# Kernel optimization log

Hardware: AMD Instinct MI355X
Metric: run time of the kernel (lower is better)

Reference implementation:

```python
import jax, jax.numpy as jnp
import numpy as np

B, L, D_PAIR, N_HEAD = 1, 320, 128, 4
EPS = 1e-5


def setup_inputs() -> dict:
    key = jax.random.key(0)
    ks = jax.random.split(key, 8)
    s = 0.05  # ~xavier scale for fan_in=128
    return {
        "pair": jax.random.normal(ks[0], (B, L, L, D_PAIR), jnp.float32),
        "norm_w": jnp.ones((D_PAIR,), jnp.float32),
        "norm_b": jnp.zeros((D_PAIR,), jnp.float32),
        "Wq": jax.random.normal(ks[1], (D_PAIR, D_PAIR), jnp.float32) * s,
        "Wk": jax.random.normal(ks[2], (D_PAIR, D_PAIR), jnp.float32) * s,
        "Wv": jax.random.normal(ks[3], (D_PAIR, D_PAIR), jnp.float32) * s,
        "Wg": jax.random.normal(ks[4], (D_PAIR, D_PAIR), jnp.float32) * s,
        "bg": jnp.zeros((D_PAIR,), jnp.float32),
        "Wo": jax.random.normal(ks[5], (D_PAIR, D_PAIR), jnp.float32) * s,
        "bo": jnp.zeros((D_PAIR,), jnp.float32),
        "Wb": jax.random.normal(ks[6], (N_HEAD, D_PAIR), jnp.float32) * s,
    }


def reference(pair, norm_w, norm_b, Wq, Wk, Wv, Wg, bg, Wo, bo, Wb):
    # Triangle attention, mode='start' (no permute). pair: (B, L, L, D)
    Bs, Ls, _, D = pair.shape
    H = Wb.shape[0]
    Dh = D // H
    scale = Dh ** -0.5

    # LayerNorm (fp32, matches torch eps=1e-5)
    mu = jnp.mean(pair, axis=-1, keepdims=True)
    var = jnp.var(pair, axis=-1, keepdims=True)
    x = (pair - mu) * jax.lax.rsqrt(var + EPS) * norm_w + norm_b

    def heads(y):
        # (B,L,L,D) -> (B,L,H,L,Dh): attention runs along the second L axis per row i
        return y.reshape(Bs, Ls, Ls, H, Dh).transpose(0, 1, 3, 2, 4)

    Q = heads(x @ Wq.T)
    K = heads(x @ Wk.T)
    V = heads(x @ Wv.T)
    g = heads(jax.nn.sigmoid(x @ Wg.T + bg))

    attn = jnp.einsum('blhid,blhjd->blhij', Q, K) * scale  # (B,L,H,L,L)
    # bias from RAW pair (pre-norm), projected to heads, broadcast over query index i
    bias = (pair @ Wb.T).transpose(0, 1, 3, 2)[:, :, :, None, :]  # (B,L,H,1,L)
    attn = jax.nn.softmax(attn + bias, axis=-1)

    out = jnp.einsum('blhij,blhjd->blhid', attn, V)  # (B,L,H,L,Dh)
    out = (g * out).transpose(0, 1, 3, 2, 4).reshape(Bs, Ls, Ls, D)
    return pair + out @ Wo.T + bo
```

## Files before the change

kernel.cpp:

```cpp
#include <hip/hip_runtime.h>

typedef unsigned short u16;
typedef unsigned int u32;
typedef __attribute__((ext_vector_type(8))) short bf16x8;
typedef __attribute__((ext_vector_type(4))) float f32x4;
typedef __attribute__((ext_vector_type(2))) unsigned int u32x2;

#define LOG2E 1.4426950408889634f

__device__ __forceinline__ u16 f2bf(float f) {
    u32 u = __float_as_uint(f);
    u += 0x7fffu + ((u >> 16) & 1u);
    return (u16)(u >> 16);
}
__device__ __forceinline__ u32 pk_bf_trunc(float hi, float lo) {
    return __builtin_amdgcn_perm(__float_as_uint(hi), __float_as_uint(lo), 0x07060302u);
}

__global__ void wconv_kernel(const float* __restrict__ Wq, const float* __restrict__ Wk,
                             const float* __restrict__ Wv, const float* __restrict__ Wg,
                             const float* __restrict__ Wo, const float* __restrict__ norm_w,
                             const float* __restrict__ norm_b, const float* __restrict__ bg,
                             u16* __restrict__ wbf, float* __restrict__ cvec) {
    int b = blockIdx.x;
    if (b < 64) {
        int idx = b * 256 + threadIdx.x;
        float w = norm_w[idx & 127];
        wbf[0 * 16384 + idx] = f2bf(Wq[idx] * w);
        wbf[1 * 16384 + idx] = f2bf(Wk[idx] * w);
        wbf[2 * 16384 + idx] = f2bf(Wv[idx] * w);
        wbf[3 * 16384 + idx] = f2bf(Wg[idx] * w);
        wbf[4 * 16384 + idx] = f2bf(Wo[idx]);
    } else {
        int m = b - 64;
        int n = threadIdx.x;
        if (n < 128) {
            const float* W = (m == 0) ? Wq : (m == 1) ? Wk : (m == 2) ? Wv : Wg;
            float c = 0.f;
#pragma unroll
            for (int k4 = 0; k4 < 32; ++k4) {
                f32x4 bb = *(const f32x4*)&norm_b[k4 * 4];
                f32x4 ww = *(const f32x4*)&W[n * 128 + k4 * 4];
                c += bb[0] * ww[0] + bb[1] * ww[1] + bb[2] * ww[2] + bb[3] * ww[3];
            }
            if (m == 3) c += bg[n];
            cvec[m * 128 + n] = c;
        }
    }
}

#define KS_OFF 9216
#define VTS_OFF 22016
#define PB_W 1152

__global__ __launch_bounds__(512, 4)
void attn_kernel(const float* __restrict__ pair,
                 const float* __restrict__ Wb,
                 const u16* __restrict__ wbf,
                 const float* __restrict__ cvec,
                 u16* __restrict__ Obf,
                 u16* __restrict__ Gg) {
    const int bid = blockIdx.x;
    const int xcd = bid & 7;
    const int s_i = bid >> 3;
    const int h = s_i & 3;
    const int l = ((s_i >> 2) << 3) | xcd;
    const int tid = threadIdx.x;
    const int wave = tid >> 6;
    const int lane = tid & 63;
    const int i_lo = lane & 15;
    const int q = lane >> 4;

    __shared__ __align__(16) u16 smem[32576];
    __shared__ __align__(16) float biasLds[320];

    const int row_g = tid >> 3;
    const int c8 = tid & 7;
    const int wrow = (wave & 3) * 16;
    const int nth_flip = wave >> 2;

    f32x4 wbv[4];
#pragma unroll
    for (int u = 0; u < 4; ++u)
        wbv[u] = *(const f32x4*)&Wb[h * 128 + c8 * 16 + u * 4];

    float cQ[2], cK[2], cV[2], cG[2];
#pragma unroll
    for (int half = 0; half < 2; ++half) {
        int n = h * 32 + half * 16 + i_lo;
        cQ[half] = cvec[0 * 128 + n];
        cK[half] = cvec[1 * 128 + n];
        cV[half] = cvec[2 * 128 + n];
        cG[half] = cvec[3 * 128 + n];
    }

    u32 qkeep[3][4];

#pragma unroll 1
    for (int t = 0; t < 5; ++t) {
        const int j0 = t * 64;
        const float* prow = pair + ((size_t)(l * 320 + j0 + row_g)) * 128 + c8 * 16;
        f32x4 pr[4];
#pragma unroll
        for (int u = 0; u < 4; ++u) pr[u] = *(const f32x4*)(prow + u * 4);

        float s = 0.f, s2 = 0.f, bd = 0.f;
#pragma unroll
        for (int u = 0; u < 4; ++u) {
            f32x4 p = pr[u];
            f32x4 wb4 = wbv[u];
            s += p[0] + p[1] + p[2] + p[3];
            s2 += p[0] * p[0] + p[1] * p[1] + p[2] * p[2] + p[3] * p[3];
            bd += p[0] * wb4[0] + p[1] * wb4[1] + p[2] * wb4[2] + p[3] * wb4[3];
        }
        s += __shfl_xor(s, 1);   s += __shfl_xor(s, 2);   s += __shfl_xor(s, 4);
        s2 += __shfl_xor(s2, 1); s2 += __shfl_xor(s2, 2); s2 += __shfl_xor(s2, 4);
        bd += __shfl_xor(bd, 1); bd += __shfl_xor(bd, 2); bd += __shfl_xor(bd, 4);
        float mu = s * 0.0078125f;
        float var = s2 * 0.0078125f - mu * mu;
        float rs = rsqrtf(var + 1e-5f);

        __syncthreads();
#pragma unroll
        for (int u = 0; u < 4; ++u) {
            f32x4 p = pr[u];
            ushort4 xv;
            xv.x = f2bf((p[0] - mu) * rs);
            xv.y = f2bf((p[1] - mu) * rs);
            xv.z = f2bf((p[2] - mu) * rs);
            xv.w = f2bf((p[3] - mu) * rs);
            *(ushort4*)&smem[row_g * 136 + c8 * 16 + u * 4] = xv;
        }
        if (c8 == 0) biasLds[j0 + row_g] = bd * LOG2E;
        __syncthreads();

        const int nth = (t & 1) ^ nth_flip;
        f32x4 acc[4];
#pragma unroll
        for (int n2 = 0; n2 < 4; ++n2) acc[n2] = (f32x4){0.f, 0.f, 0.f, 0.f};
#pragma unroll
        for (int kc = 0; kc < 4; ++kc) {
            bf16x8 a = *(const bf16x8*)&smem[(wrow + i_lo) * 136 + kc * 32 + q * 8];
#pragma unroll
            for (int n2 = 0; n2 < 4; ++n2) {
                int nt = nth * 4 + n2;
                bf16x8 wf = *(const bf16x8*)&wbf[(nt >> 1) * 16384 +
                                                 (h * 32 + (nt & 1) * 16 + i_lo) * 128 + kc * 32 + q * 8];
                acc[n2] = __builtin_amdgcn_mfma_f32_16x16x32_bf16(a, wf, acc[n2], 0, 0, 0);
            }
        }
        const int jrow = j0 + wrow + q * 4;
        if (nth == 0) {
            const int ti = t >> 1;
#pragma unroll
            for (int dd = 0; dd < 2; ++dd)
#pragma unroll
                for (int rr = 0; rr < 2; ++rr)
                    qkeep[ti][dd * 2 + rr] =
                        (u32)f2bf(acc[dd][rr * 2] + cQ[dd]) |
                        ((u32)f2bf(acc[dd][rr * 2 + 1] + cQ[dd]) << 16);
#pragma unroll
            for (int n2 = 2; n2 < 4; ++n2)
#pragma unroll
                for (int r = 0; r < 4; ++r)
                    smem[KS_OFF + (jrow + r) * 40 + (n2 & 1) * 16 + i_lo] =
                        f2bf(acc[n2][r] + cK[n2 & 1]);
        } else {
#pragma unroll
            for (int n2 = 0; n2 < 2; ++n2)
#pragma unroll
                for (int r = 0; r < 4; ++r)
                    smem[VTS_OFF + (n2 * 16 + i_lo) * 330 + jrow + r] =
                        f2bf(acc[n2][r] + cV[n2]);
#pragma unroll
            for (int n2 = 2; n2 < 4; ++n2)
#pragma unroll
                for (int r = 0; r < 4; ++r) {
                    float z = acc[n2][r] + cG[n2 & 1];
                    float g = 1.0f / (1.0f + exp2f(-z * LOG2E));
                    Gg[((size_t)((l * 4 + h) * 320 + jrow + r)) * 32 + (n2 & 1) * 16 + i_lo] = f2bf(g);
                }
        }
    }
    __syncthreads();

    const float SC = 0.17677669529663687f * LOG2E;
    const f32x4 zero4 = {0.f, 0.f, 0.f, 0.f};
    union { bf16x8 v; u32 u[4]; } onesf;
#pragma unroll
    for (int u = 0; u < 4; ++u) onesf.u[u] = 0x3F803F80u;
    u16* pb = smem + wave * PB_W;
    const int nstrip = (wave < 4) ? 3 : 2;
#pragma unroll 1
    for (int t2 = 0; t2 < nstrip; ++t2) {
        const int i0 = (wave + 8 * t2) * 16;
#pragma unroll
        for (int dd = 0; dd < 2; ++dd)
#pragma unroll
            for (int rr = 0; rr < 2; ++rr) {
                u32 v = qkeep[t2][dd * 2 + rr];
                pb[(q * 4 + rr * 2) * 40 + dd * 16 + i_lo] = (u16)v;
                pb[(q * 4 + rr * 2 + 1) * 40 + dd * 16 + i_lo] = (u16)(v >> 16);
            }
        bf16x8 qf = *(const bf16x8*)&pb[i_lo * 40 + q * 8];

        f32x4 oacc[2];
        oacc[0] = zero4; oacc[1] = zero4;
        f32x4 sacc = zero4;
#pragma unroll 1
        for (int c = 0; c < 5; ++c) {
            f32x4 sc4[4];
#pragma unroll
            for (int jt = 0; jt < 4; ++jt) {
                bf16x8 kf = *(const bf16x8*)&smem[KS_OFF + (c * 64 + jt * 16 + i_lo) * 40 + q * 8];
                sc4[jt] = __builtin_amdgcn_mfma_f32_16x16x32_bf16(kf, qf, zero4, 0, 0, 0);
            }
#pragma unroll
            for (int jt = 0; jt < 4; ++jt) {
                f32x4 b4 = *(const f32x4*)&biasLds[c * 64 + jt * 16 + q * 4];
#pragma unroll
                for (int r = 0; r < 4; ++r)
                    sc4[jt][r] = exp2f(sc4[jt][r] * SC + b4[r]);
            }
#pragma unroll
            for (int jt = 0; jt < 4; ++jt) {
                u32x2 pk;
                pk.x = pk_bf_trunc(sc4[jt][1], sc4[jt][0]);
                pk.y = pk_bf_trunc(sc4[jt][3], sc4[jt][2]);
                *(u32x2*)&pb[i_lo * 72 + jt * 16 + q * 4] = pk;
            }
#pragma unroll
            for (int kt2 = 0; kt2 < 2; ++kt2) {
                bf16x8 pf = *(const bf16x8*)&pb[i_lo * 72 + kt2 * 32 + q * 8];
                sacc = __builtin_amdgcn_mfma_f32_16x16x32_bf16(onesf.v, pf, sacc, 0, 0, 0);
#pragma unroll
                for (int mt = 0; mt < 2; ++mt) {
                    bf16x8 vf = *(const bf16x8*)&smem[VTS_OFF + (mt * 16 + i_lo) * 330 +
                                                      c * 64 + kt2 * 32 + q * 8];
                    oacc[mt] = __builtin_amdgcn_mfma_f32_16x16x32_bf16(vf, pf, oacc[mt], 0, 0, 0);
                }
            }
        }
        float rinv = 1.0f / sacc[0];
#pragma unroll
        for (int mt = 0; mt < 2; ++mt) {
            u32x2 pk;
            pk.x = pk_bf_trunc(oacc[mt][1] * rinv, oacc[mt][0] * rinv);
            pk.y = pk_bf_trunc(oacc[mt][3] * rinv, oacc[mt][2] * rinv);
            *(u32x2*)&Obf[((size_t)(l * 320 + i0 + i_lo)) * 128 + h * 32 + mt * 16 + q * 4] = pk;
        }
    }
}

__global__ __launch_bounds__(256, 4)
void outproj_kernel(const float* __restrict__ pair,
                    const float* __restrict__ bo,
                    const u16* __restrict__ Obf,
                    const u16* __restrict__ Gg,
                    const u16* __restrict__ wbf,
                    float* __restrict__ out) {
    const int tid = threadIdx.x;
    const int wave = tid >> 6;
    const int lane = tid & 63;
    const int i_lo = lane & 15;
    const int q = lane >> 4;

    __shared__ __align__(16) u16 WoLds[128 * 128];

    const int row0 = blockIdx.x * 64 + wave * 16;
    const int lidx = row0 / 320;
    const int irow = row0 - lidx * 320 + i_lo;

    union { bf16x8 v; u32 u[4]; } A[4], G[4];
#pragma unroll
    for (int kc = 0; kc < 4; ++kc) {
        A[kc].v = *(const bf16x8*)&Obf[((size_t)(row0 + i_lo)) * 128 + kc * 32 + q * 8];
        G[kc].v = *(const bf16x8*)&Gg[((size_t)((lidx * 4 + kc) * 320 + irow)) * 32 + q * 8];
    }

    const u16* Wo = wbf + 4 * 16384;
#pragma unroll
    for (int it = 0; it < 8; ++it) {
        int unit = it * 256 + tid;
        int n = unit >> 4, k8 = unit & 15;
        *(bf16x8*)&WoLds[n * 128 + ((k8 ^ (n & 15)) * 8)] = *(const bf16x8*)&Wo[unit * 8];
    }
    __syncthreads();

    bf16x8 of[4];
#pragma unroll
    for (int kc = 0; kc < 4; ++kc) {
        union { bf16x8 v; u32 u[4]; } R;
#pragma unroll
        for (int k4 = 0; k4 < 4; ++k4) {
            float lo = __uint_as_float(A[kc].u[k4] << 16) * __uint_as_float(G[kc].u[k4] << 16);
            float hi = __uint_as_float(A[kc].u[k4] & 0xffff0000u) * __uint_as_float(G[kc].u[k4] & 0xffff0000u);
            R.u[k4] = pk_bf_trunc(hi, lo);
        }
        of[kc] = R.v;
    }

    f32x4 acc[8];
#pragma unroll
    for (int nt = 0; nt < 8; ++nt) acc[nt] = (f32x4){0.f, 0.f, 0.f, 0.f};
#pragma unroll
    for (int nt = 0; nt < 8; ++nt) {
#pragma unroll
        for (int kc = 0; kc < 4; ++kc) {
            bf16x8 wf = *(const bf16x8*)&WoLds[(nt * 16 + i_lo) * 128 + (((kc * 4 + q) ^ i_lo) * 8)];
            acc[nt] = __builtin_amdgcn_mfma_f32_16x16x32_bf16(wf, of[kc], acc[nt], 0, 0, 0);
        }
    }
#pragma unroll
    for (int nt = 0; nt < 8; ++nt) {
        size_t idx = ((size_t)(row0 + i_lo)) * 128 + nt * 16 + q * 4;
        f32x4 p4 = *(const f32x4*)&pair[idx];
        f32x4 b4 = *(const f32x4*)&bo[nt * 16 + q * 4];
        f32x4 o4;
        o4[0] = acc[nt][0] + p4[0] + b4[0];
        o4[1] = acc[nt][1] + p4[1] + b4[1];
        o4[2] = acc[nt][2] + p4[2] + b4[2];
        o4[3] = acc[nt][3] + p4[3] + b4[3];
        *(f32x4*)&out[idx] = o4;
    }
}

extern "C" void kernel_launch(void* const* d_in, const int* in_sizes, int n_in,
                              void* d_out, int out_size, void* d_ws, size_t ws_size,
                              hipStream_t stream) {
    const float* pair   = (const float*)d_in[0];
    const float* norm_w = (const float*)d_in[1];
    const float* norm_b = (const float*)d_in[2];
    const float* Wq     = (const float*)d_in[3];
    const float* Wk     = (const float*)d_in[4];
    const float* Wv     = (const float*)d_in[5];
    const float* Wg     = (const float*)d_in[6];
    const float* bg     = (const float*)d_in[7];
    const float* Wo     = (const float*)d_in[8];
    const float* bo     = (const float*)d_in[9];
    const float* Wb     = (const float*)d_in[10];

    u16* wbf    = (u16*)d_ws;
    float* cvec = (float*)(wbf + 5 * 16384);
    u16* Obf    = (u16*)(cvec + 512);
    u16* Gg     = Obf + (size_t)102400 * 128;
    float* out  = (float*)d_out;

    wconv_kernel<<<68, 256, 0, stream>>>(Wq, Wk, Wv, Wg, Wo, norm_w, norm_b, bg, wbf, cvec);
    attn_kernel<<<320 * 4, 512, 0, stream>>>(pair, Wb, wbf, cvec, Obf, Gg);
    outproj_kernel<<<1600, 256, 0, stream>>>(pair, bo, Obf, Gg, wbf, out);
}
```

Before: 279.4 us.

## Process two query strips per wave sharing K/V fragments; prefetch pair residual in outproj

The attention loop now handles two 16-row query strips at once in each wave. The K fragments, bias and V fragments are loaded once and reused for both strips, and MFMA priority is raised with s_setprio so the second strip's softmax work can overlap the first strip's matrix ops. The third strip, which only waves 0-3 have, stays on the old single-strip path. In the output projection kernel the pair residual is loaded early, before the Wo LDS fill and GEMM, and launch bounds drop to 3 blocks per CU to make room for the extra registers. The trade is higher register pressure and possible loss of occupancy in exchange for fewer LDS reads and more latency hiding.

Measured after the change: 280.5 us. Within noise of the previous version (+0.4%).

```diff
diff --git a/kernel.cpp b/kernel.cpp
--- a/kernel.cpp
+++ b/kernel.cpp
@@ -190,15 +190,128 @@
 #pragma unroll
     for (int u = 0; u < 4; ++u) onesf.u[u] = 0x3F803F80u;
     u16* pb = smem + wave * PB_W;
-    const int nstrip = (wave < 4) ? 3 : 2;
+
+    {
+        const int i0A = wave * 16;
+        const int i0B = (wave + 8) * 16;
+        bf16x8 qfA, qfB;
+#pragma unroll
+        for (int dd = 0; dd < 2; ++dd)
+#pragma unroll
+            for (int rr = 0; rr < 2; ++rr) {
+                u32 v = qkeep[0][dd * 2 + rr];
+                pb[(q * 4 + rr * 2) * 40 + dd * 16 + i_lo] = (u16)v;
+                pb[(q * 4 + rr * 2 + 1) * 40 + dd * 16 + i_lo] = (u16)(v >> 16);
+            }
+        qfA = *(const bf16x8*)&pb[i_lo * 40 + q * 8];
+#pragma unroll
+        for (int dd = 0; dd < 2; ++dd)
+#pragma unroll
+            for (int rr = 0; rr < 2; ++rr) {
+                u32 v = qkeep[1][dd * 2 + rr];
+                pb[(q * 4 + rr * 2) * 40 + dd * 16 + i_lo] = (u16)v;
+                pb[(q * 4 + rr * 2 + 1) * 40 + dd * 16 + i_lo] = (u16)(v >> 16);
+            }
+        qfB = *(const bf16x8*)&pb[i_lo * 40 + q * 8];
+
+        f32x4 oaccA0 = zero4, oaccA1 = zero4, oaccB0 = zero4, oaccB1 = zero4;
+        f32x4 saccA = zero4, saccB = zero4;
 #pragma unroll 1
-    for (int t2 = 0; t2 < nstrip; ++t2) {
-        const int i0 = (wave + 8 * t2) * 16;
+        for (int c = 0; c < 5; ++c) {
+            bf16x8 kf[4];
+#pragma unroll
+            for (int jt = 0; jt < 4; ++jt)
+                kf[jt] = *(const bf16x8*)&smem[KS_OFF + (c * 64 + jt * 16 + i_lo) * 40 + q * 8];
+            f32x4 sA[4], sB[4];
+#pragma unroll
+            for (int jt = 0; jt < 4; ++jt)
+                sA[jt] = __builtin_amdgcn_mfma_f32_16x16x32_bf16(kf[jt], qfA, zero4, 0, 0, 0);
+#pragma unroll
+            for (int jt = 0; jt < 4; ++jt)
+                sB[jt] = __builtin_amdgcn_mfma_f32_16x16x32_bf16(kf[jt], qfB, zero4, 0, 0, 0);
+            f32x4 b4[4];
+#pragma unroll
+            for (int jt = 0; jt < 4; ++jt)
+                b4[jt] = *(const f32x4*)&biasLds[c * 64 + jt * 16 + q * 4];
+#pragma unroll
+            for (int jt = 0; jt < 4; ++jt)
+#pragma unroll
+                for (int r = 0; r < 4; ++r)
+                    sA[jt][r] = exp2f(sA[jt][r] * SC + b4[jt][r]);
+#pragma unroll
+            for (int jt = 0; jt < 4; ++jt) {
+                u32x2 pk;
+                pk.x = pk_bf_trunc(sA[jt][1], sA[jt][0]);
+                pk.y = pk_bf_trunc(sA[jt][3], sA[jt][2]);
+                *(u32x2*)&pb[i_lo * 72 + jt * 16 + q * 4] = pk;
+            }
+#pragma unroll
+            for (int jt = 0; jt < 4; ++jt)
+#pragma unroll
+                for (int r = 0; r < 4; ++r)
+                    sB[jt][r] = exp2f(sB[jt][r] * SC + b4[jt][r]);
+            u32 pBx[4], pBy[4];
+#pragma unroll
+            for (int jt = 0; jt < 4; ++jt) {
+                pBx[jt] = pk_bf_trunc(sB[jt][1], sB[jt][0]);
+                pBy[jt] = pk_bf_trunc(sB[jt][3], sB[jt][2]);
+            }
+            bf16x8 pfA0 = *(const bf16x8*)&pb[i_lo * 72 + 0 * 32 + q * 8];
+            bf16x8 pfA1 = *(const bf16x8*)&pb[i_lo * 72 + 1 * 32 + q * 8];
+#pragma unroll
+            for (int jt = 0; jt < 4; ++jt) {
+                u32x2 pk;
+                pk.x = pBx[jt];
+                pk.y = pBy[jt];
+                *(u32x2*)&pb[i_lo * 72 + jt * 16 + q * 4] = pk;
+            }
+            bf16x8 pfB0 = *(const bf16x8*)&pb[i_lo * 72 + 0 * 32 + q * 8];
+            bf16x8 pfB1 = *(const bf16x8*)&pb[i_lo * 72 + 1 * 32 + q * 8];
+            bf16x8 vf00 = *(const bf16x8*)&smem[VTS_OFF + (0 * 16 + i_lo) * 330 + c * 64 + 0 * 32 + q * 8];
+            bf16x8 vf01 = *(const bf16x8*)&smem[VTS_OFF + (0 * 16 + i_lo) * 330 + c * 64 + 1 * 32 + q * 8];
+            bf16x8 vf10 = *(const bf16x8*)&smem[VTS_OFF + (1 * 16 + i_lo) * 330 + c * 64 + 0 * 32 + q * 8];
+            bf16x8 vf11 = *(const bf16x8*)&smem[VTS_OFF + (1 * 16 + i_lo) * 330 + c * 64 + 1 * 32 + q * 8];
+            __builtin_amdgcn_s_setprio(1);
+            saccA = __builtin_amdgcn_mfma_f32_16x16x32_bf16(onesf.v, pfA0, saccA, 0, 0, 0);
+            saccA = __builtin_amdgcn_mfma_f32_16x16x32_bf16(onesf.v, pfA1, saccA, 0, 0, 0);
+            oaccA0 = __builtin_amdgcn_mfma_f32_16x16x32_bf16(vf00, pfA0, oaccA0, 0, 0, 0);
+            oaccA0 = __builtin_amdgcn_mfma_f32_16x16x32_bf16(vf01, pfA1, oaccA0, 0, 0, 0);
+            oaccA1 = __builtin_amdgcn_mfma_f32_16x16x32_bf16(vf10, pfA0, oaccA1, 0, 0, 0);
+            oaccA1 = __builtin_amdgcn_mfma_f32_16x16x32_bf16(vf11, pfA1, oaccA1, 0, 0, 0);
+            saccB = __builtin_amdgcn_mfma_f32_16x16x32_bf16(onesf.v, pfB0, saccB, 0, 0, 0);
+            saccB = __builtin_amdgcn_mfma_f32_16x16x32_bf16(onesf.v, pfB1, saccB, 0, 0, 0);
+            oaccB0 = __builtin_amdgcn_mfma_f32_16x16x32_bf16(vf00, pfB0, oaccB0, 0, 0, 0);
+            oaccB0 = __builtin_amdgcn_mfma_f32_16x16x32_bf16(vf01, pfB1, oaccB0, 0, 0, 0);
+            oaccB1 = __builtin_amdgcn_mfma_f32_16x16x32_bf16(vf10, pfB0, oaccB1, 0, 0, 0);
+            oaccB1 = __builtin_amdgcn_mfma_f32_16x16x32_bf16(vf11, pfB1, oaccB1, 0, 0, 0);
+            __builtin_amdgcn_s_setprio(0);
+        }
+        float rinvA = 1.0f / saccA[0];
+        float rinvB = 1.0f / saccB[0];
+        {
+            u32x2 pk;
+            pk.x = pk_bf_trunc(oaccA0[1] * rinvA, oaccA0[0] * rinvA);
+            pk.y = pk_bf_trunc(oaccA0[3] * rinvA, oaccA0[2] * rinvA);
+            *(u32x2*)&Obf[((size_t)(l * 320 + i0A + i_lo)) * 128 + h * 32 + 0 * 16 + q * 4] = pk;
+            pk.x = pk_bf_trunc(oaccA1[1] * rinvA, oaccA1[0] * rinvA);
+            pk.y = pk_bf_trunc(oaccA1[3] * rinvA, oaccA1[2] * rinvA);
+            *(u32x2*)&Obf[((size_t)(l * 320 + i0A + i_lo)) * 128 + h * 32 + 1 * 16 + q * 4] = pk;
+            pk.x = pk_bf_trunc(oaccB0[1] * rinvB, oaccB0[0] * rinvB);
+            pk.y = pk_bf_trunc(oaccB0[3] * rinvB, oaccB0[2] * rinvB);
+            *(u32x2*)&Obf[((size_t)(l * 320 + i0B + i_lo)) * 128 + h * 32 + 0 * 16 + q * 4] = pk;
+            pk.x = pk_bf_trunc(oaccB1[1] * rinvB, oaccB1[0] * rinvB);
+            pk.y = pk_bf_trunc(oaccB1[3] * rinvB, oaccB1[2] * rinvB);
+            *(u32x2*)&Obf[((size_t)(l * 320 + i0B + i_lo)) * 128 + h * 32 + 1 * 16 + q * 4] = pk;
+        }
+    }
+
+    if (wave < 4) {
+        const int i0 = (wave + 16) * 16;
 #pragma unroll
         for (int dd = 0; dd < 2; ++dd)
 #pragma unroll
             for (int rr = 0; rr < 2; ++rr) {
-                u32 v = qkeep[t2][dd * 2 + rr];
+                u32 v = qkeep[2][dd * 2 + rr];
                 pb[(q * 4 + rr * 2) * 40 + dd * 16 + i_lo] = (u16)v;
                 pb[(q * 4 + rr * 2 + 1) * 40 + dd * 16 + i_lo] = (u16)(v >> 16);
             }
@@ -252,7 +365,7 @@
     }
 }
 
-__global__ __launch_bounds__(256, 4)
+__global__ __launch_bounds__(256, 3)
 void outproj_kernel(const float* __restrict__ pair,
                     const float* __restrict__ bo,
                     const u16* __restrict__ Obf,
@@ -277,6 +390,10 @@
         A[kc].v = *(const bf16x8*)&Obf[((size_t)(row0 + i_lo)) * 128 + kc * 32 + q * 8];
         G[kc].v = *(const bf16x8*)&Gg[((size_t)((lidx * 4 + kc) * 320 + irow)) * 32 + q * 8];
     }
+    f32x4 pr[8];
+#pragma unroll
+    for (int nt = 0; nt < 8; ++nt)
+        pr[nt] = *(const f32x4*)&pair[((size_t)(row0 + i_lo)) * 128 + nt * 16 + q * 4];
 
     const u16* Wo = wbf + 4 * 16384;
 #pragma unroll
@@ -314,13 +431,12 @@
 #pragma unroll
     for (int nt = 0; nt < 8; ++nt) {
         size_t idx = ((size_t)(row0 + i_lo)) * 128 + nt * 16 + q * 4;
-        f32x4 p4 = *(const f32x4*)&pair[idx];
         f32x4 b4 = *(const f32x4*)&bo[nt * 16 + q * 4];
         f32x4 o4;
-        o4[0] = acc[nt][0] + p4[0] + b4[0];
-        o4[1] = acc[nt][1] + p4[1] + b4[1];
-        o4[2] = acc[nt][2] + p4[2] + b4[2];
-        o4[3] = acc[nt][3] + p4[3] + b4[3];
+        o4[0] = acc[nt][0] + pr[nt][0] + b4[0];
+        o4[1] = acc[nt][1] + pr[nt][1] + b4[1];
+        o4[2] = acc[nt][2] + pr[nt][2] + b4[2];
+        o4[3] = acc[nt][3] + pr[nt][3] + b4[3];
         *(f32x4*)&out[idx] = o4;
     }
 }
```

## Split fused attention kernel into separate projection and attention kernels

Applied to the files above, without the earlier changes.

Replaces the monolithic per-(row, head) attention kernel with two kernels. A projection kernel LayerNorms pair rows and computes Q, K, V^T, the gate and the bias (the bias now via an MFMA against a padded bf16 Wb), writing them to global scratch and reusing the output buffer for Q and K. A separate attention kernel then runs one 64-query block per workgroup and reads K and V directly from global memory. This removes the redundant per-head LayerNorm of each pair row and raises parallelism and occupancy, at the cost of extra global round-trips for Q, K and V. The output projection also prefetches the residual pair values early.

Result: slower. 365.0 us (+30.6%).

```diff
diff --git a/kernel.cpp b/kernel.cpp
--- a/kernel.cpp
+++ b/kernel.cpp
@@ -7,12 +7,16 @@
 typedef __attribute__((ext_vector_type(2))) unsigned int u32x2;
 
 #define LOG2E 1.4426950408889634f
+#define PB_W 1152
 
 __device__ __forceinline__ u16 f2bf(float f) {
     u32 u = __float_as_uint(f);
     u += 0x7fffu + ((u >> 16) & 1u);
     return (u16)(u >> 16);
 }
+__device__ __forceinline__ u32 pk2(float lo, float hi) {
+    return (u32)f2bf(lo) | ((u32)f2bf(hi) << 16);
+}
 __device__ __forceinline__ u32 pk_bf_trunc(float hi, float lo) {
     return __builtin_amdgcn_perm(__float_as_uint(hi), __float_as_uint(lo), 0x07060302u);
 }
@@ -21,6 +25,7 @@
                              const float* __restrict__ Wv, const float* __restrict__ Wg,
                              const float* __restrict__ Wo, const float* __restrict__ norm_w,
                              const float* __restrict__ norm_b, const float* __restrict__ bg,
+                             const float* __restrict__ Wb,
                              u16* __restrict__ wbf, float* __restrict__ cvec) {
     int b = blockIdx.x;
     if (b < 64) {
@@ -31,7 +36,7 @@
         wbf[2 * 16384 + idx] = f2bf(Wv[idx] * w);
         wbf[3 * 16384 + idx] = f2bf(Wg[idx] * w);
         wbf[4 * 16384 + idx] = f2bf(Wo[idx]);
-    } else {
+    } else if (b < 68) {
         int m = b - 64;
         int n = threadIdx.x;
         if (n < 128) {
@@ -46,213 +51,191 @@
             if (m == 3) c += bg[n];
             cvec[m * 128 + n] = c;
         }
-    }
-}
-
-#define KS_OFF 9216
-#define VTS_OFF 22016
-#define PB_W 1152
-
-__global__ __launch_bounds__(512, 4)
-void attn_kernel(const float* __restrict__ pair,
-                 const float* __restrict__ Wb,
-                 const u16* __restrict__ wbf,
-                 const float* __restrict__ cvec,
-                 u16* __restrict__ Obf,
-                 u16* __restrict__ Gg) {
+    } else {
+#pragma unroll
+        for (int e = 0; e < 8; ++e) {
+            int idx = threadIdx.x * 8 + e;
+            int n = idx >> 7;
+            wbf[5 * 16384 + idx] = (n < 4) ? f2bf(Wb[idx]) : (u16)0;
+        }
+    }
+}
+
+__global__ __launch_bounds__(256, 4)
+void proj_kernel(const float* __restrict__ pair, const u16* __restrict__ wbf,
+                 const float* __restrict__ cvec, u16* __restrict__ Qbf,
+                 u16* __restrict__ Ksb, u16* __restrict__ VTb,
+                 u16* __restrict__ Gg, float* __restrict__ biasT) {
     const int bid = blockIdx.x;
     const int xcd = bid & 7;
-    const int s_i = bid >> 3;
-    const int h = s_i & 3;
-    const int l = ((s_i >> 2) << 3) | xcd;
+    const int s = bid >> 3;
+    const int jc = s % 5;
+    const int l = (s / 5) * 8 + xcd;
     const int tid = threadIdx.x;
     const int wave = tid >> 6;
     const int lane = tid & 63;
     const int i_lo = lane & 15;
     const int q = lane >> 4;
-
-    __shared__ __align__(16) u16 smem[32576];
-    __shared__ __align__(16) float biasLds[320];
-
-    const int row_g = tid >> 3;
-    const int c8 = tid & 7;
-    const int wrow = (wave & 3) * 16;
-    const int nth_flip = wave >> 2;
-
-    f32x4 wbv[4];
-#pragma unroll
-    for (int u = 0; u < 4; ++u)
-        wbv[u] = *(const f32x4*)&Wb[h * 128 + c8 * 16 + u * 4];
-
-    float cQ[2], cK[2], cV[2], cG[2];
-#pragma unroll
-    for (int half = 0; half < 2; ++half) {
-        int n = h * 32 + half * 16 + i_lo;
-        cQ[half] = cvec[0 * 128 + n];
-        cK[half] = cvec[1 * 128 + n];
-        cV[half] = cvec[2 * 128 + n];
-        cG[half] = cvec[3 * 128 + n];
-    }
-
-    u32 qkeep[3][4];
+    const int j0 = jc * 64 + wave * 16;
+    const int row = l * 320 + j0 + i_lo;
+    const f32x4 zero4 = {0.f, 0.f, 0.f, 0.f};
+
+    f32x4 pr[8];
+    const float* pp = pair + (size_t)row * 128 + q * 8;
+#pragma unroll
+    for (int kc = 0; kc < 4; ++kc) {
+        pr[kc * 2 + 0] = *(const f32x4*)(pp + kc * 32 + 0);
+        pr[kc * 2 + 1] = *(const f32x4*)(pp + kc * 32 + 4);
+    }
+    float s1 = 0.f, s2 = 0.f;
+#pragma unroll
+    for (int u = 0; u < 8; ++u) {
+        f32x4 p = pr[u];
+        s1 += p[0] + p[1] + p[2] + p[3];
+        s2 += p[0] * p[0] + p[1] * p[1] + p[2] * p[2] + p[3] * p[3];
+    }
+    s1 += __shfl_xor(s1, 16); s1 += __shfl_xor(s1, 32);
+    s2 += __shfl_xor(s2, 16); s2 += __shfl_xor(s2, 32);
+    float mu = s1 * 0.0078125f;
+    float var = s2 * 0.0078125f - mu * mu;
+    float rs = rsqrtf(var + 1e-5f);
+
+    union { bf16x8 v; u32 u[4]; } xa[4], ra[4];
+#pragma unroll
+    for (int kc = 0; kc < 4; ++kc) {
+        f32x4 a = pr[kc * 2 + 0], b = pr[kc * 2 + 1];
+        ra[kc].u[0] = pk2(a[0], a[1]); ra[kc].u[1] = pk2(a[2], a[3]);
+        ra[kc].u[2] = pk2(b[0], b[1]); ra[kc].u[3] = pk2(b[2], b[3]);
+        xa[kc].u[0] = pk2((a[0] - mu) * rs, (a[1] - mu) * rs);
+        xa[kc].u[1] = pk2((a[2] - mu) * rs, (a[3] - mu) * rs);
+        xa[kc].u[2] = pk2((b[0] - mu) * rs, (b[1] - mu) * rs);
+        xa[kc].u[3] = pk2((b[2] - mu) * rs, (b[3] - mu) * rs);
+    }
+
+    f32x4 bacc = zero4;
+#pragma unroll
+    for (int kc = 0; kc < 4; ++kc) {
+        bf16x8 wf = *(const bf16x8*)&wbf[5 * 16384 + i_lo * 128 + kc * 32 + q * 8];
+        bacc = __builtin_amdgcn_mfma_f32_16x16x32_bf16(ra[kc].v, wf, bacc, 0, 0, 0);
+    }
+    if (i_lo < 4) {
+#pragma unroll
+        for (int r = 0; r < 4; ++r)
+            biasT[(size_t)(l * 4 + i_lo) * 320 + j0 + q * 4 + r] = bacc[r] * LOG2E;
+    }
 
 #pragma unroll 1
-    for (int t = 0; t < 5; ++t) {
-        const int j0 = t * 64;
-        const float* prow = pair + ((size_t)(l * 320 + j0 + row_g)) * 128 + c8 * 16;
-        f32x4 pr[4];
-#pragma unroll
-        for (int u = 0; u < 4; ++u) pr[u] = *(const f32x4*)(prow + u * 4);
-
-        float s = 0.f, s2 = 0.f, bd = 0.f;
-#pragma unroll
-        for (int u = 0; u < 4; ++u) {
-            f32x4 p = pr[u];
-            f32x4 wb4 = wbv[u];
-            s += p[0] + p[1] + p[2] + p[3];
-            s2 += p[0] * p[0] + p[1] * p[1] + p[2] * p[2] + p[3] * p[3];
-            bd += p[0] * wb4[0] + p[1] * wb4[1] + p[2] * wb4[2] + p[3] * wb4[3];
-        }
-        s += __shfl_xor(s, 1);   s += __shfl_xor(s, 2);   s += __shfl_xor(s, 4);
-        s2 += __shfl_xor(s2, 1); s2 += __shfl_xor(s2, 2); s2 += __shfl_xor(s2, 4);
-        bd += __shfl_xor(bd, 1); bd += __shfl_xor(bd, 2); bd += __shfl_xor(bd, 4);
-        float mu = s * 0.0078125f;
-        float var = s2 * 0.0078125f - mu * mu;
-        float rs = rsqrtf(var + 1e-5f);
-
-        __syncthreads();
-#pragma unroll
-        for (int u = 0; u < 4; ++u) {
-            f32x4 p = pr[u];
-            ushort4 xv;
-            xv.x = f2bf((p[0] - mu) * rs);
-            xv.y = f2bf((p[1] - mu) * rs);
-            xv.z = f2bf((p[2] - mu) * rs);
-            xv.w = f2bf((p[3] - mu) * rs);
-            *(ushort4*)&smem[row_g * 136 + c8 * 16 + u * 4] = xv;
-        }
-        if (c8 == 0) biasLds[j0 + row_g] = bd * LOG2E;
-        __syncthreads();
-
-        const int nth = (t & 1) ^ nth_flip;
-        f32x4 acc[4];
-#pragma unroll
-        for (int n2 = 0; n2 < 4; ++n2) acc[n2] = (f32x4){0.f, 0.f, 0.f, 0.f};
-#pragma unroll
-        for (int kc = 0; kc < 4; ++kc) {
-            bf16x8 a = *(const bf16x8*)&smem[(wrow + i_lo) * 136 + kc * 32 + q * 8];
-#pragma unroll
-            for (int n2 = 0; n2 < 4; ++n2) {
-                int nt = nth * 4 + n2;
-                bf16x8 wf = *(const bf16x8*)&wbf[(nt >> 1) * 16384 +
-                                                 (h * 32 + (nt & 1) * 16 + i_lo) * 128 + kc * 32 + q * 8];
-                acc[n2] = __builtin_amdgcn_mfma_f32_16x16x32_bf16(a, wf, acc[n2], 0, 0, 0);
+    for (int m = 0; m < 4; ++m) {
+#pragma unroll 1
+        for (int nt = 0; nt < 8; ++nt) {
+            f32x4 acc = zero4;
+#pragma unroll
+            for (int kc = 0; kc < 4; ++kc) {
+                bf16x8 wf = *(const bf16x8*)&wbf[m * 16384 + (nt * 16 + i_lo) * 128 + kc * 32 + q * 8];
+                acc = __builtin_amdgcn_mfma_f32_16x16x32_bf16(xa[kc].v, wf, acc, 0, 0, 0);
             }
-        }
-        const int jrow = j0 + wrow + q * 4;
-        if (nth == 0) {
-            const int ti = t >> 1;
-#pragma unroll
-            for (int dd = 0; dd < 2; ++dd)
-#pragma unroll
-                for (int rr = 0; rr < 2; ++rr)
-                    qkeep[ti][dd * 2 + rr] =
-                        (u32)f2bf(acc[dd][rr * 2] + cQ[dd]) |
-                        ((u32)f2bf(acc[dd][rr * 2 + 1] + cQ[dd]) << 16);
-#pragma unroll
-            for (int n2 = 2; n2 < 4; ++n2)
+            const float cv = cvec[m * 128 + nt * 16 + i_lo];
+            const int h = nt >> 1, half = nt & 1;
+            const size_t hb = (size_t)(l * 4 + h);
+            const int jr = j0 + q * 4;
+            if (m == 0) {
 #pragma unroll
                 for (int r = 0; r < 4; ++r)
-                    smem[KS_OFF + (jrow + r) * 40 + (n2 & 1) * 16 + i_lo] =
-                        f2bf(acc[n2][r] + cK[n2 & 1]);
-        } else {
-#pragma unroll
-            for (int n2 = 0; n2 < 2; ++n2)
+                    Qbf[(hb * 320 + jr + r) * 32 + half * 16 + i_lo] = f2bf(acc[r] + cv);
+            } else if (m == 1) {
 #pragma unroll
                 for (int r = 0; r < 4; ++r)
-                    smem[VTS_OFF + (n2 * 16 + i_lo) * 330 + jrow + r] =
-                        f2bf(acc[n2][r] + cV[n2]);
-#pragma unroll
-            for (int n2 = 2; n2 < 4; ++n2)
+                    Ksb[(hb * 320 + jr + r) * 32 + half * 16 + i_lo] = f2bf(acc[r] + cv);
+            } else if (m == 2) {
+                ushort4 v4;
+                v4.x = f2bf(acc[0] + cv); v4.y = f2bf(acc[1] + cv);
+                v4.z = f2bf(acc[2] + cv); v4.w = f2bf(acc[3] + cv);
+                *(ushort4*)&VTb[(hb * 32 + half * 16 + i_lo) * 320 + jr] = v4;
+            } else {
 #pragma unroll
                 for (int r = 0; r < 4; ++r) {
-                    float z = acc[n2][r] + cG[n2 & 1];
+                    float z = acc[r] + cv;
                     float g = 1.0f / (1.0f + exp2f(-z * LOG2E));
-                    Gg[((size_t)((l * 4 + h) * 320 + jrow + r)) * 32 + (n2 & 1) * 16 + i_lo] = f2bf(g);
+                    Gg[(hb * 320 + jr + r) * 32 + half * 16 + i_lo] = f2bf(g);
                 }
-        }
-    }
-    __syncthreads();
+            }
+        }
+    }
+}
+
+__global__ __launch_bounds__(256, 6)
+void attnB_kernel(const u16* __restrict__ Qbf, const u16* __restrict__ Ksb,
+                  const u16* __restrict__ VTb, const float* __restrict__ biasT,
+                  u16* __restrict__ Obf) {
+    const int bid = blockIdx.x;
+    const int xcd = bid & 7;
+    const int s = bid >> 3;
+    const int g = s % 5;
+    const int h = (s / 5) & 3;
+    const int l = (s / 20) * 8 + xcd;
+    const int tid = threadIdx.x;
+    const int wave = tid >> 6;
+    const int lane = tid & 63;
+    const int i_lo = lane & 15;
+    const int q = lane >> 4;
+    const int i0 = g * 64 + wave * 16;
+    const size_t hb = (size_t)(l * 4 + h);
+
+    __shared__ __align__(16) u16 smem[4608];
+    u16* pb = smem + wave * PB_W;
 
     const float SC = 0.17677669529663687f * LOG2E;
     const f32x4 zero4 = {0.f, 0.f, 0.f, 0.f};
     union { bf16x8 v; u32 u[4]; } onesf;
 #pragma unroll
     for (int u = 0; u < 4; ++u) onesf.u[u] = 0x3F803F80u;
-    u16* pb = smem + wave * PB_W;
-    const int nstrip = (wave < 4) ? 3 : 2;
+
+    bf16x8 qf = *(const bf16x8*)&Qbf[(hb * 320 + i0 + i_lo) * 32 + q * 8];
+
+    f32x4 oacc0 = zero4, oacc1 = zero4, sacc = zero4;
 #pragma unroll 1
-    for (int t2 = 0; t2 < nstrip; ++t2) {
-        const int i0 = (wave + 8 * t2) * 16;
-#pragma unroll
-        for (int dd = 0; dd < 2; ++dd)
-#pragma unroll
-            for (int rr = 0; rr < 2; ++rr) {
-                u32 v = qkeep[t2][dd * 2 + rr];
-                pb[(q * 4 + rr * 2) * 40 + dd * 16 + i_lo] = (u16)v;
-                pb[(q * 4 + rr * 2 + 1) * 40 + dd * 16 + i_lo] = (u16)(v >> 16);
-            }
-        bf16x8 qf = *(const bf16x8*)&pb[i_lo * 40 + q * 8];
-
-        f32x4 oacc[2];
-        oacc[0] = zero4; oacc[1] = zero4;
-        f32x4 sacc = zero4;
-#pragma unroll 1
-        for (int c = 0; c < 5; ++c) {
-            f32x4 sc4[4];
-#pragma unroll
-            for (int jt = 0; jt < 4; ++jt) {
-                bf16x8 kf = *(const bf16x8*)&smem[KS_OFF + (c * 64 + jt * 16 + i_lo) * 40 + q * 8];
-                sc4[jt] = __builtin_amdgcn_mfma_f32_16x16x32_bf16(kf, qf, zero4, 0, 0, 0);
-            }
-#pragma unroll
-            for (int jt = 0; jt < 4; ++jt) {
-                f32x4 b4 = *(const f32x4*)&biasLds[c * 64 + jt * 16 + q * 4];
-#pragma unroll
-                for (int r = 0; r < 4; ++r)
-                    sc4[jt][r] = exp2f(sc4[jt][r] * SC + b4[r]);
-            }
-#pragma unroll
-            for (int jt = 0; jt < 4; ++jt) {
-                u32x2 pk;
-                pk.x = pk_bf_trunc(sc4[jt][1], sc4[jt][0]);
-                pk.y = pk_bf_trunc(sc4[jt][3], sc4[jt][2]);
-                *(u32x2*)&pb[i_lo * 72 + jt * 16 + q * 4] = pk;
-            }
-#pragma unroll
-            for (int kt2 = 0; kt2 < 2; ++kt2) {
-                bf16x8 pf = *(const bf16x8*)&pb[i_lo * 72 + kt2 * 32 + q * 8];
-                sacc = __builtin_amdgcn_mfma_f32_16x16x32_bf16(onesf.v, pf, sacc, 0, 0, 0);
-#pragma unroll
-                for (int mt = 0; mt < 2; ++mt) {
-                    bf16x8 vf = *(const bf16x8*)&smem[VTS_OFF + (mt * 16 + i_lo) * 330 +
-                                                      c * 64 + kt2 * 32 + q * 8];
-                    oacc[mt] = __builtin_amdgcn_mfma_f32_16x16x32_bf16(vf, pf, oacc[mt], 0, 0, 0);
-                }
-            }
-        }
-        float rinv = 1.0f / sacc[0];
-#pragma unroll
-        for (int mt = 0; mt < 2; ++mt) {
+    for (int c = 0; c < 5; ++c) {
+        f32x4 sc4[4];
+#pragma unroll
+        for (int jt = 0; jt < 4; ++jt) {
+            bf16x8 kf = *(const bf16x8*)&Ksb[(hb * 320 + c * 64 + jt * 16 + i_lo) * 32 + q * 8];
+            sc4[jt] = __builtin_amdgcn_mfma_f32_16x16x32_bf16(kf, qf, zero4, 0, 0, 0);
+        }
+#pragma unroll
+        for (int jt = 0; jt < 4; ++jt) {
+            f32x4 b4 = *(const f32x4*)&biasT[hb * 320 + c * 64 + jt * 16 + q * 4];
+#pragma unroll
+            for (int r = 0; r < 4; ++r)
+                sc4[jt][r] = exp2f(sc4[jt][r] * SC + b4[r]);
+        }
+#pragma unroll
+        for (int jt = 0; jt < 4; ++jt) {
             u32x2 pk;
-            pk.x = pk_bf_trunc(oacc[mt][1] * rinv, oacc[mt][0] * rinv);
-            pk.y = pk_bf_trunc(oacc[mt][3] * rinv, oacc[mt][2] * rinv);
-            *(u32x2*)&Obf[((size_t)(l * 320 + i0 + i_lo)) * 128 + h * 32 + mt * 16 + q * 4] = pk;
-        }
-    }
-}
-
-__global__ __launch_bounds__(256, 4)
+            pk.x = pk_bf_trunc(sc4[jt][1], sc4[jt][0]);
+            pk.y = pk_bf_trunc(sc4[jt][3], sc4[jt][2]);
+            *(u32x2*)&pb[i_lo * 72 + jt * 16 + q * 4] = pk;
+        }
+#pragma unroll
+        for (int kt2 = 0; kt2 < 2; ++kt2) {
+            bf16x8 pf = *(const bf16x8*)&pb[i_lo * 72 + kt2 * 32 + q * 8];
+            sacc = __builtin_amdgcn_mfma_f32_16x16x32_bf16(onesf.v, pf, sacc, 0, 0, 0);
+            bf16x8 vf0 = *(const bf16x8*)&VTb[(hb * 32 + 0 * 16 + i_lo) * 320 + c * 64 + kt2 * 32 + q * 8];
+            bf16x8 vf1 = *(const bf16x8*)&VTb[(hb * 32 + 1 * 16 + i_lo) * 320 + c * 64 + kt2 * 32 + q * 8];
+            oacc0 = __builtin_amdgcn_mfma_f32_16x16x32_bf16(vf0, pf, oacc0, 0, 0, 0);
+            oacc1 = __builtin_amdgcn_mfma_f32_16x16x32_bf16(vf1, pf, oacc1, 0, 0, 0);
+        }
+    }
+    float rinv = 1.0f / sacc[0];
+    u32x2 pk;
+    pk.x = pk_bf_trunc(oacc0[1] * rinv, oacc0[0] * rinv);
+    pk.y = pk_bf_trunc(oacc0[3] * rinv, oacc0[2] * rinv);
+    *(u32x2*)&Obf[((size_t)(l * 320 + i0 + i_lo)) * 128 + h * 32 + 0 * 16 + q * 4] = pk;
+    pk.x = pk_bf_trunc(oacc1[1] * rinv, oacc1[0] * rinv);
+    pk.y = pk_bf_trunc(oacc1[3] * rinv, oacc1[2] * rinv);
+    *(u32x2*)&Obf[((size_t)(l * 320 + i0 + i_lo)) * 128 + h * 32 + 1 * 16 + q * 4] = pk;
+}
+
+__global__ __launch_bounds__(256, 3)
 void outproj_kernel(const float* __restrict__ pair,
                     const float* __restrict__ bo,
                     const u16* __restrict__ Obf,
@@ -277,6 +260,10 @@
         A[kc].v = *(const bf16x8*)&Obf[((size_t)(row0 + i_lo)) * 128 + kc * 32 + q * 8];
         G[kc].v = *(const bf16x8*)&Gg[((size_t)((lidx * 4 + kc) * 320 + irow)) * 32 + q * 8];
     }
+    f32x4 pr[8];
+#pragma unroll
+    for (int nt = 0; nt < 8; ++nt)
+        pr[nt] = *(const f32x4*)&pair[((size_t)(row0 + i_lo)) * 128 + nt * 16 + q * 4];
 
     const u16* Wo = wbf + 4 * 16384;
 #pragma unroll
@@ -314,13 +301,12 @@
 #pragma unroll
     for (int nt = 0; nt < 8; ++nt) {
         size_t idx = ((size_t)(row0 + i_lo)) * 128 + nt * 16 + q * 4;
-        f32x4 p4 = *(const f32x4*)&pair[idx];
         f32x4 b4 = *(const f32x4*)&bo[nt * 16 + q * 4];
         f32x4 o4;
-        o4[0] = acc[nt][0] + p4[0] + b4[0];
-        o4[1] = acc[nt][1] + p4[1] + b4[1];
-        o4[2] = acc[nt][2] + p4[2] + b4[2];
-        o4[3] = acc[nt][3] + p4[3] + b4[3];
+        o4[0] = acc[nt][0] + pr[nt][0] + b4[0];
+        o4[1] = acc[nt][1] + pr[nt][1] + b4[1];
+        o4[2] = acc[nt][2] + pr[nt][2] + b4[2];
+        o4[3] = acc[nt][3] + pr[nt][3] + b4[3];
         *(f32x4*)&out[idx] = o4;
     }
 }
@@ -340,13 +326,19 @@
     const float* bo     = (const float*)d_in[9];
     const float* Wb     = (const float*)d_in[10];
 
-    u16* wbf    = (u16*)d_ws;
-    float* cvec = (float*)(wbf + 5 * 16384);
-    u16* Obf    = (u16*)(cvec + 512);
-    u16* Gg     = Obf + (size_t)102400 * 128;
-    float* out  = (float*)d_out;
-
-    wconv_kernel<<<68, 256, 0, stream>>>(Wq, Wk, Wv, Wg, Wo, norm_w, norm_b, bg, wbf, cvec);
-    attn_kernel<<<320 * 4, 512, 0, stream>>>(pair, Wb, wbf, cvec, Obf, Gg);
+    u16*   wbf   = (u16*)d_ws;
+    float* cvec  = (float*)((char*)d_ws + 196608);
+    float* biasT = (float*)((char*)d_ws + 198656);
+    u16*   VTb   = (u16*)((char*)d_ws + 1837056);
+    u16*   Gg    = (u16*)((char*)d_ws + 28051456);
+    u16*   Obf   = (u16*)((char*)d_ws + 54265856);
+
+    u16*   Qbf   = (u16*)d_out;
+    u16*   Ksb   = (u16*)((char*)d_out + 26214400);
+    float* out   = (float*)d_out;
+
+    wconv_kernel<<<69, 256, 0, stream>>>(Wq, Wk, Wv, Wg, Wo, norm_w, norm_b, bg, Wb, wbf, cvec);
+    proj_kernel<<<1600, 256, 0, stream>>>(pair, wbf, cvec, Qbf, Ksb, VTb, Gg, biasT);
+    attnB_kernel<<<6400, 256, 0, stream>>>(Qbf, Ksb, VTb, biasT, Obf);
     outproj_kernel<<<1600, 256, 0, stream>>>(pair, bo, Obf, Gg, wbf, out);
 }
```
